# Optimization experiments

Hardware: AMD Instinct MI355X
Metric: run time of the kernel (lower is better)

## Reference

```python
import jax, jax.numpy as jnp
import numpy as np

R = 32  # voxel grid resolution
EPS = 0.0


def setup_inputs() -> dict:
    key = jax.random.key(0)
    k1, k2 = jax.random.split(key)
    B, C, N = 8, 64, 65536
    features = jax.random.normal(k1, (B, C, N), dtype=jnp.float32)
    coords = jax.random.normal(k2, (B, 3, N), dtype=jnp.float32)
    return {"features": features, "coords": coords}


def _voxelize_coords(coords):
    # coords: [B, 3, N] -> normalized coords [B,3,N] and voxel indices [B,3,N]
    coords = jax.lax.stop_gradient(coords)  # torch: coords.detach()
    nc = coords - coords.mean(axis=2, keepdims=True)
    # normalize=True branch
    norms = jnp.linalg.norm(nc, axis=1, keepdims=True)        # [B,1,N]
    max_norm = norms.max(axis=2, keepdims=True)               # [B,1,1]
    nc = nc / (max_norm * 2.0 + EPS) + 0.5
    nc = jnp.clip(nc * R, 0.0, R - 1)
    vox = jnp.round(nc).astype(jnp.int32)                     # [B,3,N]
    return nc, vox


def _avg_voxelize(features, vox):
    # features: [B, C, N]; vox: [B, 3, N] int -> [B, C, R, R, R]
    B, C, N = features.shape
    flat = vox[:, 0] * (R * R) + vox[:, 1] * R + vox[:, 2]    # [B, N]
    seg = (flat + jnp.arange(B, dtype=jnp.int32)[:, None] * (R ** 3)).reshape(-1)
    feats = features.transpose(0, 2, 1).reshape(B * N, C)      # [B*N, C]
    sums = jax.ops.segment_sum(feats, seg, num_segments=B * R ** 3)          # [B*R^3, C]
    counts = jax.ops.segment_sum(jnp.ones((B * N,), features.dtype), seg,
                                 num_segments=B * R ** 3)                     # [B*R^3]
    avg = sums / jnp.maximum(counts, 1.0)[:, None]
    return avg.reshape(B, R ** 3, C).transpose(0, 2, 1).reshape(B, C, R, R, R)


def reference(features, coords):
    nc, vox = _voxelize_coords(coords)
    out = _avg_voxelize(features, vox)
    return out, nc
```

## Files before the change

kernel.cpp:

```cpp
#include <hip/hip_runtime.h>
#include <hip/hip_bf16.h>
#include <cstdint>

static constexpr int B_  = 8;
static constexpr int C_  = 64;
static constexpr int N_  = 65536;
static constexpr int Rr  = 32;
static constexpr int R3  = Rr * Rr * Rr;
static constexpr int PBLK  = 16;
static constexpr int PBLKM = 64;
static constexpr int PTS_PER_BLK  = N_ / PBLK;
static constexpr int PTS_PER_BLKM = N_ / PBLKM;

__device__ __forceinline__ float bf2f(unsigned short u) {
    union { unsigned int i; float f; } x;
    x.i = ((unsigned int)u) << 16;
    return x.f;
}
__device__ __forceinline__ unsigned short f2bf(float f) {
    __hip_bfloat16 h = (__hip_bfloat16)f;
    return *reinterpret_cast<unsigned short*>(&h);
}

__global__ void pmean_zero_kernel(const float* __restrict__ coords,
                                  float* __restrict__ pmean,
                                  int4* __restrict__ counts4,
                                  int* __restrict__ n_occ) {
    if (blockIdx.x >= B_ * 3 * PBLK) {
        const int zb = blockIdx.x - B_ * 3 * PBLK;
        counts4[zb * 256 + threadIdx.x] = make_int4(0, 0, 0, 0);
        if (zb == 0 && threadIdx.x == 0) *n_occ = 0;
        return;
    }
    const int blk = blockIdx.x & (PBLK - 1);
    const int ba  = blockIdx.x / PBLK;
    const float4* p = (const float4*)(coords + (size_t)ba * N_ + (size_t)blk * PTS_PER_BLK);
    float s = 0.f;
    #pragma unroll
    for (int k = 0; k < PTS_PER_BLK / 4 / 256; ++k) {
        float4 v = p[k * 256 + threadIdx.x];
        s += (v.x + v.y) + (v.z + v.w);
    }
    #pragma unroll
    for (int off = 32; off >= 1; off >>= 1) s += __shfl_down(s, off, 64);
    __shared__ float sm[4];
    if ((threadIdx.x & 63) == 0) sm[threadIdx.x >> 6] = s;
    __syncthreads();
    if (threadIdx.x == 0) pmean[blockIdx.x] = sm[0] + sm[1] + sm[2] + sm[3];
}

__global__ void partial_max_kernel(const float* __restrict__ coords,
                                   const float* __restrict__ pmean,
                                   float* __restrict__ pmax) {
    const int blk = blockIdx.x & (PBLKM - 1);
    const int b   = blockIdx.x / PBLKM;
    __shared__ float msh[3];
    if (threadIdx.x == 0) {
        #pragma unroll
        for (int a = 0; a < 3; ++a) {
            float t = 0.f;
            #pragma unroll
            for (int k = 0; k < PBLK; ++k) t += pmean[(b * 3 + a) * PBLK + k];
            msh[a] = t / (float)N_;
        }
    }
    __syncthreads();
    const float mx = msh[0], my = msh[1], mz = msh[2];
    const float4* px = (const float4*)(coords + (size_t)b * 3 * N_ + (size_t)blk * PTS_PER_BLKM);
    const float4* py = px + N_ / 4;
    const float4* pz = px + 2 * (N_ / 4);
    const int i = threadIdx.x;
    float4 x = px[i], y = py[i], z = pz[i];
    float m = 0.f;
    {
        float x0 = x.x - mx, y0 = y.x - my, z0 = z.x - mz;
        float x1 = x.y - mx, y1 = y.y - my, z1 = z.y - mz;
        float x2 = x.z - mx, y2 = y.z - my, z2 = z.z - mz;
        float x3 = x.w - mx, y3 = y.w - my, z3 = z.w - mz;
        m = fmaxf(m, x0 * x0 + y0 * y0 + z0 * z0);
        m = fmaxf(m, x1 * x1 + y1 * y1 + z1 * z1);
        m = fmaxf(m, x2 * x2 + y2 * y2 + z2 * z2);
        m = fmaxf(m, x3 * x3 + y3 * y3 + z3 * z3);
    }
    #pragma unroll
    for (int off = 32; off >= 1; off >>= 1) m = fmaxf(m, __shfl_down(m, off, 64));
    __shared__ float sm[4];
    if ((threadIdx.x & 63) == 0) sm[threadIdx.x >> 6] = m;
    __syncthreads();
    if (threadIdx.x == 0)
        pmax[blockIdx.x] = fmaxf(fmaxf(sm[0], sm[1]), fmaxf(sm[2], sm[3]));
}

__global__ void voxelize_kernel(const float* __restrict__ coords,
                                const float* __restrict__ pmean,
                                const float* __restrict__ pmax,
                                float* __restrict__ nc_out,
                                int* __restrict__ flat_out,
                                int* __restrict__ counts) {
    const int idx = blockIdx.x * blockDim.x + threadIdx.x;
    const int b = idx >> 16;
    const int n = idx & (N_ - 1);
    __shared__ float par[4];
    if (threadIdx.x == 0) {
        #pragma unroll
        for (int a = 0; a < 3; ++a) {
            float t = 0.f;
            #pragma unroll
            for (int k = 0; k < PBLK; ++k) t += pmean[(b * 3 + a) * PBLK + k];
            par[a] = t / (float)N_;
        }
        float mm = 0.f;
        #pragma unroll
        for (int k = 0; k < PBLKM; ++k) mm = fmaxf(mm, pmax[b * PBLKM + k]);
        par[3] = 2.0f * sqrtf(mm);
    }
    __syncthreads();
    const float* pc = coords + (size_t)b * 3 * N_;
    const float denom = par[3];
    int flat = 0;
    #pragma unroll
    for (int a = 0; a < 3; ++a) {
        float v = (pc[(size_t)a * N_ + n] - par[a]) / denom + 0.5f;
        v = v * (float)Rr;
        v = fminf(fmaxf(v, 0.0f), (float)(Rr - 1));
        nc_out[(size_t)b * 3 * N_ + (size_t)a * N_ + n] = v;
        flat = flat * Rr + (int)rintf(v);
    }
    flat_out[idx] = flat;
    atomicAdd(&counts[b * R3 + flat], 1);
}

__global__ void scan_compact_kernel(const int* __restrict__ counts,
                                    int* __restrict__ cursor,
                                    int4* __restrict__ clist,
                                    int* __restrict__ n_occ) {
    const int b = blockIdx.x;
    const int t = threadIdx.x;
    const int lane = t & 63, wv = t >> 6;
    constexpr int PER = R3 / 1024;
    int local[PER];
    const int4* c4 = (const int4*)(counts + b * R3);
    int s = 0, nz = 0;
    #pragma unroll
    for (int k = 0; k < PER / 4; ++k) {
        const int4 v = c4[t * (PER / 4) + k];
        local[k * 4 + 0] = v.x; local[k * 4 + 1] = v.y;
        local[k * 4 + 2] = v.z; local[k * 4 + 3] = v.w;
        s  += v.x + v.y + v.z + v.w;
        nz += (v.x > 0) + (v.y > 0) + (v.z > 0) + (v.w > 0);
    }
    const int s_own = s, nz_own = nz;
    #pragma unroll
    for (int off = 1; off < 64; off <<= 1) {
        const int vs = __shfl_up(s, off, 64);
        const int vn = __shfl_up(nz, off, 64);
        if (lane >= off) { s += vs; nz += vn; }
    }
    __shared__ int wsum[16], wnz[16], woffs[16], woffn[16];
    __shared__ int basesh;
    if (lane == 63) { wsum[wv] = s; wnz[wv] = nz; }
    __syncthreads();
    if (t < 16) {
        const int as = wsum[t], an = wnz[t];
        int is = as, in_ = an;
        #pragma unroll
        for (int off = 1; off < 16; off <<= 1) {
            const int vs = __shfl_up(is, off, 16);
            const int vn = __shfl_up(in_, off, 16);
            if (t >= off) { is += vs; in_ += vn; }
        }
        woffs[t] = is - as;
        woffn[t] = in_ - an;
        if (t == 15) basesh = atomicAdd(n_occ, in_);
    }
    __syncthreads();
    int run  = woffs[wv] + (s - s_own);
    int slot = basesh + woffn[wv] + (nz - nz_own);
    int* cur = cursor + b * R3 + t * PER;
    #pragma unroll
    for (int k = 0; k < PER; ++k) {
        cur[k] = run;
        if (local[k] > 0) clist[slot++] = make_int4(b * R3 + t * PER + k, run, local[k], 0);
        run += local[k];
    }
}

__global__ void sorted_transpose_ids_kernel(const float* __restrict__ features,
                                            const int* __restrict__ flat,
                                            int* __restrict__ cursor,
                                            __hip_bfloat16* __restrict__ ftS) {
    const int tile = blockIdx.x & 1023;
    const int b    = blockIdx.x >> 10;
    const int n0   = tile * 64;
    __shared__ unsigned short tileS[64][66];
    __shared__ int pos_s[64];
    const int t = threadIdx.x;
    if (t < 64) {
        const int f = flat[b * N_ + n0 + t];
        pos_s[t] = atomicAdd(&cursor[b * R3 + f], 1);
    }
    const int g  = t & 15;
    const int c0 = t >> 4;
    #pragma unroll
    for (int it = 0; it < 4; ++it) {
        const int c = it * 16 + c0;
        const float4 v = *(const float4*)(features + ((size_t)b * C_ + c) * N_ + n0 + g * 4);
        ushort4 u;
        u.x = f2bf(v.x); u.y = f2bf(v.y); u.z = f2bf(v.z); u.w = f2bf(v.w);
        *(ushort4*)&tileS[c][g * 4] = u;
    }
    __syncthreads();
    #pragma unroll
    for (int p = 0; p < 2; ++p) {
        const int oi = p * 256 + t;
        const int j  = oi >> 3;
        const int o  = oi & 7;
        const int cb = o * 8;
        unsigned int w0 = (unsigned int)tileS[cb + 0][j] | ((unsigned int)tileS[cb + 1][j] << 16);
        unsigned int w1 = (unsigned int)tileS[cb + 2][j] | ((unsigned int)tileS[cb + 3][j] << 16);
        unsigned int w2 = (unsigned int)tileS[cb + 4][j] | ((unsigned int)tileS[cb + 5][j] << 16);
        unsigned int w3 = (unsigned int)tileS[cb + 6][j] | ((unsigned int)tileS[cb + 7][j] << 16);
        *(uint4*)((unsigned short*)ftS + ((size_t)b * N_ + pos_s[j]) * C_ + cb) =
            make_uint4(w0, w1, w2, w3);
    }
}

__global__ void voxel_sum_compact_kernel(const __hip_bfloat16* __restrict__ ftS,
                                         const int4* __restrict__ clist,
                                         const int* __restrict__ n_occ,
                                         float* __restrict__ acc) {
    const int lane = threadIdx.x & 63;
    const int gw = blockIdx.x * (blockDim.x >> 6) + (threadIdx.x >> 6);
    const int nw = gridDim.x * (blockDim.x >> 6);
    const int tot = *n_occ;
    const int sub = lane >> 4;
    const int g   = lane & 15;
    for (int e = gw; e < tot; e += nw) {
        const int4 ent = clist[e];
        const int wid = ent.x, start = ent.y, cnt = ent.z;
        const int b = wid >> 15;
        const unsigned short* base =
            (const unsigned short*)ftS + ((size_t)b * N_ + start) * C_ + g * 4;
        float a0 = 0.f, a1 = 0.f, a2 = 0.f, a3 = 0.f;
        for (int t = sub; t < cnt; t += 4) {
            const ushort4 u = *(const ushort4*)(base + (size_t)t * C_);
            a0 += bf2f(u.x); a1 += bf2f(u.y); a2 += bf2f(u.z); a3 += bf2f(u.w);
        }
        #pragma unroll
        for (int off = 16; off <= 32; off <<= 1) {
            a0 += __shfl_xor(a0, off, 64);
            a1 += __shfl_xor(a1, off, 64);
            a2 += __shfl_xor(a2, off, 64);
            a3 += __shfl_xor(a3, off, 64);
        }
        if (sub == 0) {
            *(float4*)(acc + (size_t)wid * C_ + g * 4) = make_float4(a0, a1, a2, a3);
        }
    }
}

__global__ void transpose_finalize_kernel(const float* __restrict__ acc,
                                          const int* __restrict__ counts,
                                          float* __restrict__ out) {
    const int chunk = blockIdx.x;
    const int b  = chunk >> 9;
    const int v0 = (chunk & 511) * 64;
    __shared__ float tile[64][65];
    __shared__ float cnt_s[64];
    __shared__ int   occ[64];
    const int lane = threadIdx.x & 63, row0 = threadIdx.x >> 6;
    if (threadIdx.x < 64) {
        const int c = counts[b * R3 + v0 + threadIdx.x];
        occ[threadIdx.x]   = c;
        cnt_s[threadIdx.x] = fmaxf((float)c, 1.0f);
    }
    __syncthreads();
    #pragma unroll
    for (int it = 0; it < 16; ++it) {
        const int vi = row0 + it * 4;
        tile[vi][lane] = occ[vi] ? acc[((size_t)(b * R3 + v0 + vi)) * C_ + lane] : 0.f;
    }
    __syncthreads();
    #pragma unroll
    for (int it = 0; it < 16; ++it) {
        const int c = row0 + it * 4;
        out[((size_t)b * C_ + c) * R3 + v0 + lane] = tile[lane][c] / cnt_s[lane];
    }
}

__global__ void mean_kernel(const float* __restrict__ coords,
                            float* __restrict__ mean_out) {
    const int ba = blockIdx.x;
    const float* p = coords + (size_t)ba * N_;
    float s = 0.f;
    for (int i = threadIdx.x; i < N_; i += blockDim.x) s += p[i];
    #pragma unroll
    for (int off = 32; off >= 1; off >>= 1) s += __shfl_down(s, off, 64);
    __shared__ float sm[4];
    if ((threadIdx.x & 63) == 0) sm[threadIdx.x >> 6] = s;
    __syncthreads();
    if (threadIdx.x == 0) mean_out[ba] = (sm[0] + sm[1] + sm[2] + sm[3]) / (float)N_;
}

__global__ void maxnorm_kernel(const float* __restrict__ coords,
                               const float* __restrict__ mean,
                               float* __restrict__ maxn) {
    const int b = blockIdx.x;
    const float* p = coords + (size_t)b * 3 * N_;
    const float mx = mean[b * 3 + 0], my = mean[b * 3 + 1], mz = mean[b * 3 + 2];
    float m = 0.f;
    for (int i = threadIdx.x; i < N_; i += blockDim.x) {
        const float x = p[i] - mx, y = p[N_ + i] - my, z = p[2 * N_ + i] - mz;
        m = fmaxf(m, x * x + y * y + z * z);
    }
    #pragma unroll
    for (int off = 32; off >= 1; off >>= 1) m = fmaxf(m, __shfl_down(m, off, 64));
    __shared__ float sm[16];
    if ((threadIdx.x & 63) == 0) sm[threadIdx.x >> 6] = m;
    __syncthreads();
    if (threadIdx.x == 0) {
        float t = sm[0];
        const int nw = blockDim.x >> 6;
        for (int w = 1; w < nw; ++w) t = fmaxf(t, sm[w]);
        maxn[b] = sqrtf(t);
    }
}

__global__ void scatter_kernel(const float* __restrict__ coords,
                               const float* __restrict__ features,
                               const float* __restrict__ mean,
                               const float* __restrict__ maxn,
                               float* __restrict__ out,
                               float* __restrict__ nc_out,
                               float* __restrict__ counts) {
    const int idx = blockIdx.x * blockDim.x + threadIdx.x;
    if (idx >= B_ * N_) return;
    const int b = idx >> 16;
    const int n = idx & (N_ - 1);
    const float* pc = coords + (size_t)b * 3 * N_;
    const float denom = 2.0f * maxn[b];
    int flat = 0;
    #pragma unroll
    for (int a = 0; a < 3; ++a) {
        float v = (pc[(size_t)a * N_ + n] - mean[b * 3 + a]) / denom + 0.5f;
        v = v * (float)Rr;
        v = fminf(fmaxf(v, 0.0f), (float)(Rr - 1));
        nc_out[(size_t)b * 3 * N_ + (size_t)a * N_ + n] = v;
        flat = flat * Rr + (int)rintf(v);
    }
    atomicAdd(&counts[b * R3 + flat], 1.0f);
    const float* pf = features + (size_t)b * C_ * N_ + n;
    float* po = out + (size_t)b * C_ * R3 + flat;
    #pragma unroll 4
    for (int c = 0; c < C_; ++c) atomicAdd(po + (size_t)c * R3, pf[(size_t)c * N_]);
}

__global__ void finalize_kernel(float* __restrict__ out,
                                const float* __restrict__ counts) {
    const int idx = blockIdx.x * blockDim.x + threadIdx.x;
    if (idx >= B_ * C_ * R3) return;
    const int b = idx / (C_ * R3);
    const int v = idx & (R3 - 1);
    out[idx] = out[idx] / fmaxf(counts[b * R3 + v], 1.0f);
}

extern "C" void kernel_launch(void* const* d_in, const int* in_sizes, int n_in,
                              void* d_out, int out_size, void* d_ws, size_t ws_size,
                              hipStream_t stream) {
    const float* features = (const float*)d_in[0];
    const float* coords   = (const float*)d_in[1];

    float* out    = (float*)d_out;
    float* nc_out = out + (size_t)B_ * C_ * R3;

    const size_t accB   = (size_t)B_ * R3 * C_ * sizeof(float);
    const size_t cntB   = (size_t)B_ * R3 * sizeof(int);
    const size_t curB   = cntB;
    const size_t flatB  = (size_t)B_ * N_ * sizeof(int);
    const size_t clistB = (size_t)B_ * R3 * sizeof(int4);
    const size_t smallB = 16384;
    const size_t ftsB   = (size_t)B_ * N_ * C_ * sizeof(__hip_bfloat16);

    const size_t need = accB + cntB + curB + flatB + clistB + smallB + ftsB;
    const int pts = B_ * N_;

    if (ws_size >= need) {
        char* w = (char*)d_ws;
        float* acc    = (float*)w;                 w += accB;
        int*   counts = (int*)w;                   w += cntB;
        int*   cursor = (int*)w;                   w += curB;
        int*   flat   = (int*)w;                   w += flatB;
        int4*  clist  = (int4*)w;                  w += clistB;
        int*   n_occ  = (int*)w;
        float* pmean  = (float*)(w + 16);
        float* pmax   = pmean + B_ * 3 * PBLK;
        w += smallB;
        __hip_bfloat16* ftS = (__hip_bfloat16*)w;

        pmean_zero_kernel<<<B_ * 3 * PBLK + 256, 256, 0, stream>>>(
            coords, pmean, (int4*)counts, n_occ);
        partial_max_kernel<<<B_ * PBLKM, 256, 0, stream>>>(coords, pmean, pmax);
        voxelize_kernel<<<pts / 256, 256, 0, stream>>>(
            coords, pmean, pmax, nc_out, flat, counts);
        scan_compact_kernel<<<B_, 1024, 0, stream>>>(counts, cursor, clist, n_occ);
        sorted_transpose_ids_kernel<<<B_ * (N_ / 64), 256, 0, stream>>>(
            features, flat, cursor, ftS);
        voxel_sum_compact_kernel<<<1024, 256, 0, stream>>>(ftS, clist, n_occ, acc);
        transpose_finalize_kernel<<<B_ * (R3 / 64), 256, 0, stream>>>(acc, counts, out);
    } else {
        float* counts = (float*)d_ws;
        float* mean   = counts + (size_t)B_ * R3;
        float* maxn   = mean + B_ * 3;

        hipMemsetAsync(d_out, 0, (size_t)B_ * C_ * R3 * sizeof(float), stream);
        hipMemsetAsync(d_ws, 0, ((size_t)B_ * R3 + B_ * 3 + B_) * sizeof(float), stream);

        mean_kernel<<<B_ * 3, 256, 0, stream>>>(coords, mean);
        maxnorm_kernel<<<B_, 1024, 0, stream>>>(coords, mean, maxn);
        scatter_kernel<<<(pts + 255) / 256, 256, 0, stream>>>(
            coords, features, mean, maxn, out, nc_out, counts);
        finalize_kernel<<<(B_ * C_ * R3 + 255) / 256, 256, 0, stream>>>(out, counts);
    }
}
```

Before: 184.4 us.

## Transpose features in natural order in first kernel, gather via sorted index list

The feature transpose to bf16 point-major layout now runs in the first kernel, fused with the coordinate mean and zeroing, so it no longer waits on voxelization and the scan. A separate kernel scatters only point indices into voxel-sorted order, and the summation kernel gathers feature rows indirectly through that index list. This takes the large feature pass off the dependent chain, at the cost of uncoalesced random 8-byte gathers in the sum kernel and an extra index array.

Result: slower. 233.6 us (+26.7%).

```diff
diff --git a/kernel.cpp b/kernel.cpp
--- a/kernel.cpp
+++ b/kernel.cpp
@@ -11,6 +11,7 @@
 static constexpr int PBLKM = 64;
 static constexpr int PTS_PER_BLK  = N_ / PBLK;
 static constexpr int PTS_PER_BLKM = N_ / PBLKM;
+static constexpr int NTILES = B_ * (N_ / 64);
 
 __device__ __forceinline__ float bf2f(unsigned short u) {
     union { unsigned int i; float f; } x;
@@ -22,31 +23,65 @@
     return *reinterpret_cast<unsigned short*>(&h);
 }
 
-__global__ void pmean_zero_kernel(const float* __restrict__ coords,
-                                  float* __restrict__ pmean,
-                                  int4* __restrict__ counts4,
-                                  int* __restrict__ n_occ) {
-    if (blockIdx.x >= B_ * 3 * PBLK) {
-        const int zb = blockIdx.x - B_ * 3 * PBLK;
-        counts4[zb * 256 + threadIdx.x] = make_int4(0, 0, 0, 0);
-        if (zb == 0 && threadIdx.x == 0) *n_occ = 0;
+__global__ void ftn_pmean_zero_kernel(const float* __restrict__ features,
+                                      const float* __restrict__ coords,
+                                      float* __restrict__ pmean,
+                                      int4* __restrict__ counts4,
+                                      int* __restrict__ n_occ,
+                                      __hip_bfloat16* __restrict__ ftN) {
+    int bid = blockIdx.x;
+    const int t = threadIdx.x;
+    if (bid < NTILES) {
+        const int b  = bid >> 10;
+        const int n0 = (bid & 1023) << 6;
+        __shared__ unsigned short tileS[64][66];
+        const int g  = t & 15;
+        const int c0 = t >> 4;
+        #pragma unroll
+        for (int it = 0; it < 4; ++it) {
+            const int c = it * 16 + c0;
+            const float4 v = *(const float4*)(features + ((size_t)b * C_ + c) * N_ + n0 + g * 4);
+            ushort4 u;
+            u.x = f2bf(v.x); u.y = f2bf(v.y); u.z = f2bf(v.z); u.w = f2bf(v.w);
+            *(ushort4*)&tileS[c][g * 4] = u;
+        }
+        __syncthreads();
+        #pragma unroll
+        for (int p = 0; p < 2; ++p) {
+            const int oi = p * 256 + t;
+            const int j  = oi >> 3;
+            const int cb = (oi & 7) * 8;
+            unsigned int w0 = (unsigned int)tileS[cb + 0][j] | ((unsigned int)tileS[cb + 1][j] << 16);
+            unsigned int w1 = (unsigned int)tileS[cb + 2][j] | ((unsigned int)tileS[cb + 3][j] << 16);
+            unsigned int w2 = (unsigned int)tileS[cb + 4][j] | ((unsigned int)tileS[cb + 5][j] << 16);
+            unsigned int w3 = (unsigned int)tileS[cb + 6][j] | ((unsigned int)tileS[cb + 7][j] << 16);
+            *(uint4*)((unsigned short*)ftN + ((size_t)b * N_ + n0 + j) * C_ + cb) =
+                make_uint4(w0, w1, w2, w3);
+        }
         return;
     }
-    const int blk = blockIdx.x & (PBLK - 1);
-    const int ba  = blockIdx.x / PBLK;
-    const float4* p = (const float4*)(coords + (size_t)ba * N_ + (size_t)blk * PTS_PER_BLK);
-    float s = 0.f;
-    #pragma unroll
-    for (int k = 0; k < PTS_PER_BLK / 4 / 256; ++k) {
-        float4 v = p[k * 256 + threadIdx.x];
-        s += (v.x + v.y) + (v.z + v.w);
-    }
-    #pragma unroll
-    for (int off = 32; off >= 1; off >>= 1) s += __shfl_down(s, off, 64);
-    __shared__ float sm[4];
-    if ((threadIdx.x & 63) == 0) sm[threadIdx.x >> 6] = s;
-    __syncthreads();
-    if (threadIdx.x == 0) pmean[blockIdx.x] = sm[0] + sm[1] + sm[2] + sm[3];
+    bid -= NTILES;
+    if (bid < B_ * 3 * PBLK) {
+        const int blk = bid & (PBLK - 1);
+        const int ba  = bid / PBLK;
+        const float4* p = (const float4*)(coords + (size_t)ba * N_ + (size_t)blk * PTS_PER_BLK);
+        float s = 0.f;
+        #pragma unroll
+        for (int k = 0; k < PTS_PER_BLK / 4 / 256; ++k) {
+            float4 v = p[k * 256 + t];
+            s += (v.x + v.y) + (v.z + v.w);
+        }
+        #pragma unroll
+        for (int off = 32; off >= 1; off >>= 1) s += __shfl_down(s, off, 64);
+        __shared__ float sm[4];
+        if ((t & 63) == 0) sm[t >> 6] = s;
+        __syncthreads();
+        if (t == 0) pmean[bid] = sm[0] + sm[1] + sm[2] + sm[3];
+        return;
+    }
+    bid -= B_ * 3 * PBLK;
+    counts4[bid * 256 + t] = make_int4(0, 0, 0, 0);
+    if (bid == 0 && t == 0) *n_occ = 0;
 }
 
 __global__ void partial_max_kernel(const float* __restrict__ coords,
@@ -185,50 +220,23 @@
     }
 }
 
-__global__ void sorted_transpose_ids_kernel(const float* __restrict__ features,
-                                            const int* __restrict__ flat,
-                                            int* __restrict__ cursor,
-                                            __hip_bfloat16* __restrict__ ftS) {
-    const int tile = blockIdx.x & 1023;
-    const int b    = blockIdx.x >> 10;
-    const int n0   = tile * 64;
-    __shared__ unsigned short tileS[64][66];
-    __shared__ int pos_s[64];
-    const int t = threadIdx.x;
-    if (t < 64) {
-        const int f = flat[b * N_ + n0 + t];
-        pos_s[t] = atomicAdd(&cursor[b * R3 + f], 1);
-    }
-    const int g  = t & 15;
-    const int c0 = t >> 4;
-    #pragma unroll
-    for (int it = 0; it < 4; ++it) {
-        const int c = it * 16 + c0;
-        const float4 v = *(const float4*)(features + ((size_t)b * C_ + c) * N_ + n0 + g * 4);
-        ushort4 u;
-        u.x = f2bf(v.x); u.y = f2bf(v.y); u.z = f2bf(v.z); u.w = f2bf(v.w);
-        *(ushort4*)&tileS[c][g * 4] = u;
-    }
-    __syncthreads();
-    #pragma unroll
-    for (int p = 0; p < 2; ++p) {
-        const int oi = p * 256 + t;
-        const int j  = oi >> 3;
-        const int o  = oi & 7;
-        const int cb = o * 8;
-        unsigned int w0 = (unsigned int)tileS[cb + 0][j] | ((unsigned int)tileS[cb + 1][j] << 16);
-        unsigned int w1 = (unsigned int)tileS[cb + 2][j] | ((unsigned int)tileS[cb + 3][j] << 16);
-        unsigned int w2 = (unsigned int)tileS[cb + 4][j] | ((unsigned int)tileS[cb + 5][j] << 16);
-        unsigned int w3 = (unsigned int)tileS[cb + 6][j] | ((unsigned int)tileS[cb + 7][j] << 16);
-        *(uint4*)((unsigned short*)ftS + ((size_t)b * N_ + pos_s[j]) * C_ + cb) =
-            make_uint4(w0, w1, w2, w3);
-    }
-}
-
-__global__ void voxel_sum_compact_kernel(const __hip_bfloat16* __restrict__ ftS,
-                                         const int4* __restrict__ clist,
-                                         const int* __restrict__ n_occ,
-                                         float* __restrict__ acc) {
+__global__ void scatter_ids_kernel(const int* __restrict__ flat,
+                                   int* __restrict__ cursor,
+                                   int* __restrict__ sorted_n) {
+    const int idx = blockIdx.x * blockDim.x + threadIdx.x;
+    if (idx >= B_ * N_) return;
+    const int b = idx >> 16;
+    const int n = idx & (N_ - 1);
+    const int f = flat[idx];
+    const int p = atomicAdd(&cursor[b * R3 + f], 1);
+    sorted_n[b * N_ + p] = n;
+}
+
+__global__ void voxel_sum_gather_kernel(const __hip_bfloat16* __restrict__ ftN,
+                                        const int* __restrict__ sorted_n,
+                                        const int4* __restrict__ clist,
+                                        const int* __restrict__ n_occ,
+                                        float* __restrict__ acc) {
     const int lane = threadIdx.x & 63;
     const int gw = blockIdx.x * (blockDim.x >> 6) + (threadIdx.x >> 6);
     const int nw = gridDim.x * (blockDim.x >> 6);
@@ -239,11 +247,12 @@
         const int4 ent = clist[e];
         const int wid = ent.x, start = ent.y, cnt = ent.z;
         const int b = wid >> 15;
-        const unsigned short* base =
-            (const unsigned short*)ftS + ((size_t)b * N_ + start) * C_ + g * 4;
+        const int* sn = sorted_n + b * N_ + start;
+        const unsigned short* fb = (const unsigned short*)ftN + (size_t)b * N_ * C_ + g * 4;
         float a0 = 0.f, a1 = 0.f, a2 = 0.f, a3 = 0.f;
         for (int t = sub; t < cnt; t += 4) {
-            const ushort4 u = *(const ushort4*)(base + (size_t)t * C_);
+            const int n = sn[t];
+            const ushort4 u = *(const ushort4*)(fb + (size_t)n * C_);
             a0 += bf2f(u.x); a1 += bf2f(u.y); a2 += bf2f(u.z); a3 += bf2f(u.w);
         }
         #pragma unroll
@@ -377,35 +386,36 @@
     const size_t cntB   = (size_t)B_ * R3 * sizeof(int);
     const size_t curB   = cntB;
     const size_t flatB  = (size_t)B_ * N_ * sizeof(int);
+    const size_t snB    = flatB;
     const size_t clistB = (size_t)B_ * R3 * sizeof(int4);
     const size_t smallB = 16384;
-    const size_t ftsB   = (size_t)B_ * N_ * C_ * sizeof(__hip_bfloat16);
-
-    const size_t need = accB + cntB + curB + flatB + clistB + smallB + ftsB;
+    const size_t ftnB   = (size_t)B_ * N_ * C_ * sizeof(__hip_bfloat16);
+
+    const size_t need = accB + cntB + curB + flatB + snB + clistB + smallB + ftnB;
     const int pts = B_ * N_;
 
     if (ws_size >= need) {
         char* w = (char*)d_ws;
-        float* acc    = (float*)w;                 w += accB;
-        int*   counts = (int*)w;                   w += cntB;
-        int*   cursor = (int*)w;                   w += curB;
-        int*   flat   = (int*)w;                   w += flatB;
-        int4*  clist  = (int4*)w;                  w += clistB;
-        int*   n_occ  = (int*)w;
-        float* pmean  = (float*)(w + 16);
-        float* pmax   = pmean + B_ * 3 * PBLK;
+        float* acc      = (float*)w;               w += accB;
+        int*   counts   = (int*)w;                 w += cntB;
+        int*   cursor   = (int*)w;                 w += curB;
+        int*   flat     = (int*)w;                 w += flatB;
+        int*   sorted_n = (int*)w;                 w += snB;
+        int4*  clist    = (int4*)w;                w += clistB;
+        int*   n_occ    = (int*)w;
+        float* pmean    = (float*)(w + 16);
+        float* pmax     = pmean + B_ * 3 * PBLK;
         w += smallB;
-        __hip_bfloat16* ftS = (__hip_bfloat16*)w;
-
-        pmean_zero_kernel<<<B_ * 3 * PBLK + 256, 256, 0, stream>>>(
-            coords, pmean, (int4*)counts, n_occ);
+        __hip_bfloat16* ftN = (__hip_bfloat16*)w;
+
+        ftn_pmean_zero_kernel<<<NTILES + B_ * 3 * PBLK + 256, 256, 0, stream>>>(
+            features, coords, pmean, (int4*)counts, n_occ, ftN);
         partial_max_kernel<<<B_ * PBLKM, 256, 0, stream>>>(coords, pmean, pmax);
         voxelize_kernel<<<pts / 256, 256, 0, stream>>>(
             coords, pmean, pmax, nc_out, flat, counts);
         scan_compact_kernel<<<B_, 1024, 0, stream>>>(counts, cursor, clist, n_occ);
-        sorted_transpose_ids_kernel<<<B_ * (N_ / 64), 256, 0, stream>>>(
-            features, flat, cursor, ftS);
-        voxel_sum_compact_kernel<<<1024, 256, 0, stream>>>(ftS, clist, n_occ, acc);
+        scatter_ids_kernel<<<pts / 256, 256, 0, stream>>>(flat, cursor, sorted_n);
+        voxel_sum_gather_kernel<<<1024, 256, 0, stream>>>(ftN, sorted_n, clist, n_occ, acc);
         transpose_finalize_kernel<<<B_ * (R3 / 64), 256, 0, stream>>>(acc, counts, out);
     } else {
         float* counts = (float*)d_ws;
```
